# Kernel optimization log

Hardware: AMD Instinct MI355X
Metric: run time of the kernel (lower is better)

## Reference

```python
import jax, jax.numpy as jnp
import numpy as np


def setup_inputs() -> dict:
    key = jax.random.key(0)
    ks = jax.random.split(key, 5)
    B, C, H, W = 4, 256, 64, 64
    Cq = C // 8
    x = jax.random.normal(ks[0], (B, C, H, W), dtype=jnp.float32)
    Wq = jax.random.normal(ks[1], (Cq, C), dtype=jnp.float32) * (1.0 / np.sqrt(C))
    Wk = jax.random.normal(ks[2], (Cq, C), dtype=jnp.float32) * (1.0 / np.sqrt(C))
    Wv = jax.random.normal(ks[3], (C, C), dtype=jnp.float32) * (1.0 / np.sqrt(C))
    bq = jnp.zeros((Cq,), dtype=jnp.float32)
    bk = jnp.zeros((Cq,), dtype=jnp.float32)
    bv = jnp.zeros((C,), dtype=jnp.float32)
    gamma = jnp.ones((1,), dtype=jnp.float32)
    return {"x": x, "Wq": Wq, "bq": bq, "Wk": Wk, "bk": bk, "Wv": Wv, "bv": bv, "gamma": gamma}


def reference(x, Wq, bq, Wk, bk, Wv, bv, gamma):
    B, C, H, W = x.shape
    N = H * W
    xf = x.reshape(B, C, N)                      # (B, C, N)
    # 1x1 convs == per-pixel linear projections over channels
    q = jnp.einsum('dc,bcn->bdn', Wq, xf) + bq[None, :, None]   # (B, C/8, N)
    k = jnp.einsum('dc,bcn->bdn', Wk, xf) + bk[None, :, None]   # (B, C/8, N)
    v = jnp.einsum('dc,bcn->bdn', Wv, xf) + bv[None, :, None]   # (B, C,   N)
    # attention: note original has NO 1/sqrt(d) scaling
    scores = jnp.einsum('bdn,bdm->bnm', q, k)     # (B, N, N)
    attn = jax.nn.softmax(scores, axis=-1)
    out = jnp.einsum('bnm,bdm->bnd', attn, v)     # (B, N, C)
    out = out.transpose(0, 2, 1).reshape(B, C, H, W)
    return gamma * out + x
```

## Files before the change

kernel.cpp:

```cpp
#include <hip/hip_runtime.h>

#define BATCH 4
#define CH    256
#define DQ    32
#define NPIX  4096
#define LOG2E 1.4426950408889634f

typedef unsigned short u16;
typedef unsigned int   u32;
typedef __attribute__((ext_vector_type(8))) short short8;
typedef __attribute__((ext_vector_type(16))) float f32x16;

#if defined(__has_builtin)
#if __has_builtin(__builtin_amdgcn_exp2f)
#define EXP2F(x) __builtin_amdgcn_exp2f(x)
#else
#define EXP2F(x) __expf((x) * 0.6931471805599453f)
#endif
#else
#define EXP2F(x) __expf((x) * 0.6931471805599453f)
#endif

__device__ __forceinline__ float b2f(u32 u) {
  union { u32 i; float f; } v; v.i = (u & 0xffffu) << 16; return v.f;
}
__device__ __forceinline__ u16 f2b(float f) {
  union { float f; u32 i; } v; v.f = f;
  u32 x = v.i; x += 0x7fffu + ((x >> 16) & 1u);
  return (u16)(x >> 16);
}
__device__ __forceinline__ u32 pack_hi16(float lo, float hi) {
  union { float f; u32 i; } a, b; a.f = lo; b.f = hi;
  return __builtin_amdgcn_perm(b.i, a.i, 0x07060302u);
}

__global__ __launch_bounds__(256) void wconv(
    const float* __restrict__ Wq, const float* __restrict__ Wk,
    const float* __restrict__ Wv, u16* __restrict__ wsz, u16* __restrict__ wsz_lo)
{
  const int blk = blockIdx.x;
  const int jt = blk >> 4, kk = blk & 15;
  #pragma unroll
  for (int rep = 0; rep < 2; ++rep) {
    const int idx = rep * 256 + threadIdx.x;
    const int j = idx >> 4, el = idx & 15, e = kk * 16 + el;
    const float* Wsrc = (jt == 0) ? Wq : (jt == 1) ? Wk : Wv;
    const int row = (jt <= 1) ? j : (jt - 2) * 32 + j;
    float v = Wsrc[(size_t)row * CH + e];
    if (jt == 0) v *= LOG2E;
    const u16 hi = f2b(v);
    const int o = (((jt * 16 + kk) * 2 + (el >> 3)) * 32 + j) * 8 + (el & 7);
    wsz[o] = hi;
    if (jt < 2) wsz_lo[o] = f2b(v - b2f(hi));
  }
}

__global__ __launch_bounds__(64, 4) void proj(
    const float* __restrict__ x,
    const u16* __restrict__ wsz, const u16* __restrict__ wsz_lo,
    const float* __restrict__ bq, const float* __restrict__ bk, const float* __restrict__ bv,
    u16* __restrict__ q_t, u16* __restrict__ k_t, u16* __restrict__ v_swz)
{
  const int nt = blockIdx.x, jt = blockIdx.y, b = blockIdx.z;
  const int lane = threadIdx.x & 63, hl = lane >> 5, l31 = lane & 31;
  const int n = nt * 32 + l31;

  const float* xb = x + (size_t)b * CH * NPIX + n;

  if (jt <= 1) {
    f32x16 a0, a1, a2;
    #pragma unroll
    for (int r = 0; r < 16; ++r) { a0[r] = 0.f; a1[r] = 0.f; a2[r] = 0.f; }
    for (int kk = 0; kk < 16; ++kk) {
      const int wo = ((jt * 16 + kk) * 2 + hl) * 256 + l31 * 8;
      const short8 Ah = *(const short8*)&wsz[wo];
      const short8 Al = *(const short8*)&wsz_lo[wo];
      float xv[8];
      #pragma unroll
      for (int j = 0; j < 8; ++j)
        xv[j] = xb[(size_t)(kk * 16 + hl * 8 + j) * NPIX];
      union { u32 u[4]; short8 s; } Bh, Bl;
      #pragma unroll
      for (int j2 = 0; j2 < 4; ++j2) {
        const u16 h0 = f2b(xv[2 * j2]),     h1 = f2b(xv[2 * j2 + 1]);
        const u16 l0 = f2b(xv[2 * j2] - b2f(h0));
        const u16 l1 = f2b(xv[2 * j2 + 1] - b2f(h1));
        Bh.u[j2] = (u32)h0 | ((u32)h1 << 16);
        Bl.u[j2] = (u32)l0 | ((u32)l1 << 16);
      }
      a0 = __builtin_amdgcn_mfma_f32_32x32x16_bf16(Ah, Bh.s, a0, 0, 0, 0);
      a1 = __builtin_amdgcn_mfma_f32_32x32x16_bf16(Ah, Bl.s, a1, 0, 0, 0);
      a2 = __builtin_amdgcn_mfma_f32_32x32x16_bf16(Al, Bh.s, a2, 0, 0, 0);
    }
    u16* dst = (jt == 0) ? q_t : k_t;
    const float* bias = (jt == 0) ? bq : bk;
    const float bscale = (jt == 0) ? LOG2E : 1.0f;
    #pragma unroll
    for (int r = 0; r < 16; ++r) {
      const int d = (r & 3) + 8 * (r >> 2) + 4 * hl;
      dst[((size_t)b * NPIX + n) * DQ + d] =
        f2b((a0[r] + a1[r]) + (a2[r] + bias[d] * bscale));
    }
  } else {
    f32x16 a0, a1;
    #pragma unroll
    for (int r = 0; r < 16; ++r) { a0[r] = 0.f; a1[r] = 0.f; }
    for (int kk = 0; kk < 16; kk += 2) {
      #pragma unroll
      for (int par = 0; par < 2; ++par) {
        const int k2 = kk + par;
        const short8 Ah = *(const short8*)&wsz[((jt * 16 + k2) * 2 + hl) * 256 + l31 * 8];
        float xv[8];
        #pragma unroll
        for (int j = 0; j < 8; ++j)
          xv[j] = xb[(size_t)(k2 * 16 + hl * 8 + j) * NPIX];
        union { u32 u[4]; short8 s; } Bh;
        #pragma unroll
        for (int j2 = 0; j2 < 4; ++j2)
          Bh.u[j2] = (u32)f2b(xv[2 * j2]) | ((u32)f2b(xv[2 * j2 + 1]) << 16);
        if (par == 0) a0 = __builtin_amdgcn_mfma_f32_32x32x16_bf16(Ah, Bh.s, a0, 0, 0, 0);
        else          a1 = __builtin_amdgcn_mfma_f32_32x32x16_bf16(Ah, Bh.s, a1, 0, 0, 0);
      }
    }
    const int ctv = jt - 2;
    const int kc = (l31 >> 4) & 1, h3 = (l31 >> 3) & 1, j8 = l31 & 7;
    u16* dst = v_swz + (((((size_t)b * 128 + nt) * 8 + ctv) * 2 + kc) * 2 + h3) * 256 + j8;
    #pragma unroll
    for (int r = 0; r < 16; ++r) {
      const int c5 = (r & 3) + 8 * (r >> 2) + 4 * hl;
      dst[c5 * 8] = f2b(a0[r] + a1[r] + bv[ctv * 32 + c5]);
    }
  }
}

__global__ __launch_bounds__(512, 1) void attn(
    const u16* __restrict__ q_t, const u16* __restrict__ k_t,
    const u16* __restrict__ v_swz, const float* __restrict__ x,
    const float* __restrict__ gamma, float* __restrict__ out)
{
  const int b = blockIdx.y, t = threadIdx.x;
  const int w = t >> 6, lane = t & 63, hl = lane >> 5, l31 = lane & 31;
  const int mq = w >> 1, ch = w & 1;
  const int n0 = blockIdx.x * 64;

  __shared__ float cbuf[16384];
  __shared__ float lbuf[8][2][64];

  short8 qf[2][2];
  #pragma unroll
  for (int nt = 0; nt < 2; ++nt)
    #pragma unroll
    for (int kd = 0; kd < 2; ++kd)
      qf[nt][kd] = *(const short8*)(q_t + ((size_t)b * NPIX + n0 + nt * 32 + l31) * DQ + kd * 16 + hl * 8);

  f32x16 acc[8];
  #pragma unroll
  for (int a = 0; a < 8; ++a)
    #pragma unroll
    for (int r = 0; r < 16; ++r) acc[a][r] = 0.f;
  float lrun[2] = {0.f, 0.f};

  const u16* kb = k_t + (size_t)b * NPIX * DQ;
  const u16* vb = v_swz + (size_t)b * 128 * 8192;

  for (int cc = 0; cc < 32; ++cc) {
    const int mc = mq * 32 + cc;

    const u16* kp = kb + (size_t)(mc * 32 + l31) * DQ + hl * 8;
    const short8 kf0 = *(const short8*)(kp);
    const short8 kf1 = *(const short8*)(kp + 16);

    short8 av[4][2];
    const u16* vp = vb + (size_t)mc * 8192 + (size_t)hl * 256 + l31 * 8;
    #pragma unroll
    for (int ct = 0; ct < 4; ++ct)
      #pragma unroll
      for (int kc = 0; kc < 2; ++kc)
        av[ct][kc] = *(const short8*)(vp + (((ch * 4 + ct) * 2 + kc) * 2) * 256);

    union { uint4 u; short8 s; } bu[2][2];
    #pragma unroll
    for (int nt = 0; nt < 2; ++nt) {
      f32x16 st;
      #pragma unroll
      for (int r = 0; r < 16; ++r) st[r] = 0.f;
      st = __builtin_amdgcn_mfma_f32_32x32x16_bf16(kf0, qf[nt][0], st, 0, 0, 0);
      st = __builtin_amdgcn_mfma_f32_32x32x16_bf16(kf1, qf[nt][1], st, 0, 0, 0);
      u32 pk[4][2];
      #pragma unroll
      for (int g = 0; g < 4; ++g) {
        const float e0 = EXP2F(st[4 * g + 0]);
        const float e1 = EXP2F(st[4 * g + 1]);
        const float e2 = EXP2F(st[4 * g + 2]);
        const float e3 = EXP2F(st[4 * g + 3]);
        lrun[nt] += (e0 + e1) + (e2 + e3);
        pk[g][0] = pack_hi16(e0, e1);
        pk[g][1] = pack_hi16(e2, e3);
      }
      #pragma unroll
      for (int kc = 0; kc < 2; ++kc) {
        const u32 s0 = hl ? pk[2 * kc][0] : pk[2 * kc + 1][0];
        const u32 s1 = hl ? pk[2 * kc][1] : pk[2 * kc + 1][1];
        const u32 r0 = (u32)__shfl_xor((int)s0, 32);
        const u32 r1 = (u32)__shfl_xor((int)s1, 32);
        bu[nt][kc].u.x = hl ? r0 : pk[2 * kc][0];
        bu[nt][kc].u.y = hl ? r1 : pk[2 * kc][1];
        bu[nt][kc].u.z = hl ? pk[2 * kc + 1][0] : r0;
        bu[nt][kc].u.w = hl ? pk[2 * kc + 1][1] : r1;
      }
    }

    #pragma unroll
    for (int kc = 0; kc < 2; ++kc)
      #pragma unroll
      for (int ct = 0; ct < 4; ++ct)
        #pragma unroll
        for (int nt = 0; nt < 2; ++nt)
          acc[nt * 4 + ct] =
            __builtin_amdgcn_mfma_f32_32x32x16_bf16(av[ct][kc], bu[nt][kc].s, acc[nt * 4 + ct], 0, 0, 0);
  }

  lbuf[w][0][lane] = lrun[0];
  lbuf[w][1][lane] = lrun[1];

  #pragma unroll
  for (int nt = 0; nt < 2; ++nt) {
    if (mq == 1 || mq == 3) {
      const int slot = (ch * 2 + (mq >> 1)) * 4096;
      #pragma unroll
      for (int ct = 0; ct < 4; ++ct)
        #pragma unroll
        for (int r = 0; r < 16; ++r)
          cbuf[slot + (ct * 16 + r) * 64 + lane] = acc[nt * 4 + ct][r];
    }
    __syncthreads();
    if (mq == 0 || mq == 2) {
      const int slot = (ch * 2 + (mq >> 1)) * 4096;
      #pragma unroll
      for (int ct = 0; ct < 4; ++ct)
        #pragma unroll
        for (int r = 0; r < 16; ++r)
          acc[nt * 4 + ct][r] += cbuf[slot + (ct * 16 + r) * 64 + lane];
    }
    __syncthreads();
    if (mq == 2) {
      const int slot = ch * 2 * 4096;
      #pragma unroll
      for (int ct = 0; ct < 4; ++ct)
        #pragma unroll
        for (int r = 0; r < 16; ++r)
          cbuf[slot + (ct * 16 + r) * 64 + lane] = acc[nt * 4 + ct][r];
    }
    __syncthreads();
    if (mq == 0) {
      const int slot = ch * 2 * 4096;
      #pragma unroll
      for (int ct = 0; ct < 4; ++ct)
        #pragma unroll
        for (int r = 0; r < 16; ++r)
          acc[nt * 4 + ct][r] += cbuf[slot + (ct * 16 + r) * 64 + lane];
    }
    __syncthreads();
  }

  if (mq == 0) {
    const float g = gamma[0];
    #pragma unroll
    for (int nt = 0; nt < 2; ++nt) {
      float l = 0.f;
      #pragma unroll
      for (int ww = 0; ww < 8; ++ww) l += lbuf[ww][nt][lane];
      l += __shfl_xor(l, 32);
      const float linv = 2.0f / l;
      #pragma unroll
      for (int ct = 0; ct < 4; ++ct)
        #pragma unroll
        for (int r = 0; r < 16; ++r) {
          const int c = (ch * 4 + ct) * 32 + (r & 3) + 8 * (r >> 2) + 4 * hl;
          const size_t idx = ((size_t)b * CH + c) * NPIX + n0 + nt * 32 + l31;
          out[idx] = g * acc[nt * 4 + ct][r] * linv + x[idx];
        }
    }
  }
}

extern "C" void kernel_launch(void* const* d_in, const int* in_sizes, int n_in,
                              void* d_out, int out_size, void* d_ws, size_t ws_size,
                              hipStream_t stream) {
  const float* x  = (const float*)d_in[0];
  const float* Wq = (const float*)d_in[1];
  const float* bq = (const float*)d_in[2];
  const float* Wk = (const float*)d_in[3];
  const float* bk = (const float*)d_in[4];
  const float* Wv = (const float*)d_in[5];
  const float* bv = (const float*)d_in[6];
  const float* gm = (const float*)d_in[7];
  float* out = (float*)d_out;

  const size_t qk_e = (size_t)BATCH * NPIX * DQ;
  const size_t v_e  = (size_t)BATCH * NPIX * CH;
  const size_t w_e  = 10 * 16 * 2 * 32 * 8;
  const size_t wl_e = 2 * 16 * 2 * 32 * 8;
  const size_t need = (2 * qk_e + v_e + w_e + wl_e) * sizeof(u16);
  if (ws_size < need) return;

  u16* q_t    = (u16*)d_ws;
  u16* k_t    = q_t + qk_e;
  u16* v_swz  = k_t + qk_e;
  u16* wsz    = v_swz + v_e;
  u16* wsz_lo = wsz + w_e;

  wconv<<<dim3(160), 256, 0, stream>>>(Wq, Wk, Wv, wsz, wsz_lo);
  proj <<<dim3(NPIX / 32, 10, BATCH), 64, 0, stream>>>(x, wsz, wsz_lo, bq, bk, bv, q_t, k_t, v_swz);
  attn <<<dim3(NPIX / 64, BATCH), 512, 0, stream>>>(q_t, k_t, v_swz, x, gm, out);
}
```

Measured before the change: 184.8 us.

## Stage x tile in LDS once per block in projection; split V loads in attention

The projection kernel now launches one 256-thread block per pixel tile and batch instead of ten 64-thread blocks. It loads the x tile once with float4 reads, converts it to bf16 hi/lo in shared memory, and all four waves reuse it for the Q, K and V outputs. This removes the tenfold redundant strided global reads of x and repeated bf16 conversion, at the cost of LDS use and fewer, heavier blocks. In the attention kernel the V fragment loads are split into two halves interleaved with the MFMAs, lowering register pressure.

```diff
diff --git a/kernel.cpp b/kernel.cpp
--- a/kernel.cpp
+++ b/kernel.cpp
@@ -55,42 +55,52 @@
   }
 }
 
-__global__ __launch_bounds__(64, 4) void proj(
+__global__ __launch_bounds__(256) void proj(
     const float* __restrict__ x,
     const u16* __restrict__ wsz, const u16* __restrict__ wsz_lo,
     const float* __restrict__ bq, const float* __restrict__ bk, const float* __restrict__ bv,
     u16* __restrict__ q_t, u16* __restrict__ k_t, u16* __restrict__ v_swz)
 {
-  const int nt = blockIdx.x, jt = blockIdx.y, b = blockIdx.z;
-  const int lane = threadIdx.x & 63, hl = lane >> 5, l31 = lane & 31;
-  const int n = nt * 32 + l31;
-
-  const float* xb = x + (size_t)b * CH * NPIX + n;
-
-  if (jt <= 1) {
+  const int nt = blockIdx.x, b = blockIdx.y;
+  const int n0 = nt * 32;
+  const int t = threadIdx.x;
+  const int w = t >> 6, hl = (t >> 5) & 1, l31 = t & 31;
+
+  __shared__ __align__(16) u16 xh[32 * 264];
+  __shared__ __align__(16) u16 xl[32 * 264];
+
+  #pragma unroll
+  for (int p = 0; p < 8; ++p) {
+    const int e = p * 32 + (t >> 3), n4 = (t & 7) * 4;
+    const float4 v4 = *(const float4*)&x[((size_t)b * CH + e) * NPIX + n0 + n4];
+    const float vv[4] = {v4.x, v4.y, v4.z, v4.w};
+    #pragma unroll
+    for (int jj = 0; jj < 4; ++jj) {
+      const u16 hi = f2b(vv[jj]);
+      xh[(n4 + jj) * 264 + e] = hi;
+      xl[(n4 + jj) * 264 + e] = f2b(vv[jj] - b2f(hi));
+    }
+  }
+  __syncthreads();
+
+  const int n = n0 + l31;
+
+  if (w <= 1) {
+    const int jt = w;
     f32x16 a0, a1, a2;
     #pragma unroll
     for (int r = 0; r < 16; ++r) { a0[r] = 0.f; a1[r] = 0.f; a2[r] = 0.f; }
+    #pragma unroll
     for (int kk = 0; kk < 16; ++kk) {
       const int wo = ((jt * 16 + kk) * 2 + hl) * 256 + l31 * 8;
       const short8 Ah = *(const short8*)&wsz[wo];
       const short8 Al = *(const short8*)&wsz_lo[wo];
-      float xv[8];
-      #pragma unroll
-      for (int j = 0; j < 8; ++j)
-        xv[j] = xb[(size_t)(kk * 16 + hl * 8 + j) * NPIX];
-      union { u32 u[4]; short8 s; } Bh, Bl;
-      #pragma unroll
-      for (int j2 = 0; j2 < 4; ++j2) {
-        const u16 h0 = f2b(xv[2 * j2]),     h1 = f2b(xv[2 * j2 + 1]);
-        const u16 l0 = f2b(xv[2 * j2] - b2f(h0));
-        const u16 l1 = f2b(xv[2 * j2 + 1] - b2f(h1));
-        Bh.u[j2] = (u32)h0 | ((u32)h1 << 16);
-        Bl.u[j2] = (u32)l0 | ((u32)l1 << 16);
-      }
-      a0 = __builtin_amdgcn_mfma_f32_32x32x16_bf16(Ah, Bh.s, a0, 0, 0, 0);
-      a1 = __builtin_amdgcn_mfma_f32_32x32x16_bf16(Ah, Bl.s, a1, 0, 0, 0);
-      a2 = __builtin_amdgcn_mfma_f32_32x32x16_bf16(Al, Bh.s, a2, 0, 0, 0);
+      const int xo = l31 * 264 + kk * 16 + hl * 8;
+      const short8 Bh = *(const short8*)&xh[xo];
+      const short8 Bl = *(const short8*)&xl[xo];
+      a0 = __builtin_amdgcn_mfma_f32_32x32x16_bf16(Ah, Bh, a0, 0, 0, 0);
+      a1 = __builtin_amdgcn_mfma_f32_32x32x16_bf16(Ah, Bl, a1, 0, 0, 0);
+      a2 = __builtin_amdgcn_mfma_f32_32x32x16_bf16(Al, Bh, a2, 0, 0, 0);
     }
     u16* dst = (jt == 0) ? q_t : k_t;
     const float* bias = (jt == 0) ? bq : bk;
@@ -102,33 +112,29 @@
         f2b((a0[r] + a1[r]) + (a2[r] + bias[d] * bscale));
     }
   } else {
-    f32x16 a0, a1;
-    #pragma unroll
-    for (int r = 0; r < 16; ++r) { a0[r] = 0.f; a1[r] = 0.f; }
-    for (int kk = 0; kk < 16; kk += 2) {
-      #pragma unroll
-      for (int par = 0; par < 2; ++par) {
-        const int k2 = kk + par;
-        const short8 Ah = *(const short8*)&wsz[((jt * 16 + k2) * 2 + hl) * 256 + l31 * 8];
-        float xv[8];
-        #pragma unroll
-        for (int j = 0; j < 8; ++j)
-          xv[j] = xb[(size_t)(k2 * 16 + hl * 8 + j) * NPIX];
-        union { u32 u[4]; short8 s; } Bh;
-        #pragma unroll
-        for (int j2 = 0; j2 < 4; ++j2)
-          Bh.u[j2] = (u32)f2b(xv[2 * j2]) | ((u32)f2b(xv[2 * j2 + 1]) << 16);
-        if (par == 0) a0 = __builtin_amdgcn_mfma_f32_32x32x16_bf16(Ah, Bh.s, a0, 0, 0, 0);
-        else          a1 = __builtin_amdgcn_mfma_f32_32x32x16_bf16(Ah, Bh.s, a1, 0, 0, 0);
+    #pragma unroll
+    for (int ci = 0; ci < 4; ++ci) {
+      const int ctv = (w - 2) * 4 + ci;
+      const int jt = 2 + ctv;
+      f32x16 a0, a1;
+      #pragma unroll
+      for (int r = 0; r < 16; ++r) { a0[r] = 0.f; a1[r] = 0.f; }
+      #pragma unroll
+      for (int kk = 0; kk < 16; kk += 2) {
+        const short8 Ah0 = *(const short8*)&wsz[((jt * 16 + kk) * 2 + hl) * 256 + l31 * 8];
+        const short8 Bh0 = *(const short8*)&xh[l31 * 264 + kk * 16 + hl * 8];
+        const short8 Ah1 = *(const short8*)&wsz[((jt * 16 + kk + 1) * 2 + hl) * 256 + l31 * 8];
+        const short8 Bh1 = *(const short8*)&xh[l31 * 264 + (kk + 1) * 16 + hl * 8];
+        a0 = __builtin_amdgcn_mfma_f32_32x32x16_bf16(Ah0, Bh0, a0, 0, 0, 0);
+        a1 = __builtin_amdgcn_mfma_f32_32x32x16_bf16(Ah1, Bh1, a1, 0, 0, 0);
       }
-    }
-    const int ctv = jt - 2;
-    const int kc = (l31 >> 4) & 1, h3 = (l31 >> 3) & 1, j8 = l31 & 7;
-    u16* dst = v_swz + (((((size_t)b * 128 + nt) * 8 + ctv) * 2 + kc) * 2 + h3) * 256 + j8;
-    #pragma unroll
-    for (int r = 0; r < 16; ++r) {
-      const int c5 = (r & 3) + 8 * (r >> 2) + 4 * hl;
-      dst[c5 * 8] = f2b(a0[r] + a1[r] + bv[ctv * 32 + c5]);
+      const int kc = (l31 >> 4) & 1, h3 = (l31 >> 3) & 1, j8 = l31 & 7;
+      u16* dst = v_swz + (((((size_t)b * 128 + nt) * 8 + ctv) * 2 + kc) * 2 + h3) * 256 + j8;
+      #pragma unroll
+      for (int r = 0; r < 16; ++r) {
+        const int c5 = (r & 3) + 8 * (r >> 2) + 4 * hl;
+        dst[c5 * 8] = f2b(a0[r] + a1[r] + bv[ctv * 32 + c5]);
+      }
     }
   }
 }
@@ -170,13 +176,11 @@
     const short8 kf0 = *(const short8*)(kp);
     const short8 kf1 = *(const short8*)(kp + 16);
 
-    short8 av[4][2];
     const u16* vp = vb + (size_t)mc * 8192 + (size_t)hl * 256 + l31 * 8;
+    short8 av[4];
     #pragma unroll
     for (int ct = 0; ct < 4; ++ct)
-      #pragma unroll
-      for (int kc = 0; kc < 2; ++kc)
-        av[ct][kc] = *(const short8*)(vp + (((ch * 4 + ct) * 2 + kc) * 2) * 256);
+      av[ct] = *(const short8*)(vp + (((ch * 4 + ct) * 2 + 0) * 2) * 256);
 
     union { uint4 u; short8 s; } bu[2][2];
     #pragma unroll
@@ -211,13 +215,21 @@
     }
 
     #pragma unroll
-    for (int kc = 0; kc < 2; ++kc)
-      #pragma unroll
-      for (int ct = 0; ct < 4; ++ct)
-        #pragma unroll
-        for (int nt = 0; nt < 2; ++nt)
-          acc[nt * 4 + ct] =
-            __builtin_amdgcn_mfma_f32_32x32x16_bf16(av[ct][kc], bu[nt][kc].s, acc[nt * 4 + ct], 0, 0, 0);
+    for (int ct = 0; ct < 4; ++ct)
+      #pragma unroll
+      for (int nt = 0; nt < 2; ++nt)
+        acc[nt * 4 + ct] =
+          __builtin_amdgcn_mfma_f32_32x32x16_bf16(av[ct], bu[nt][0].s, acc[nt * 4 + ct], 0, 0, 0);
+
+    #pragma unroll
+    for (int ct = 0; ct < 4; ++ct)
+      av[ct] = *(const short8*)(vp + (((ch * 4 + ct) * 2 + 1) * 2) * 256);
+    #pragma unroll
+    for (int ct = 0; ct < 4; ++ct)
+      #pragma unroll
+      for (int nt = 0; nt < 2; ++nt)
+        acc[nt * 4 + ct] =
+          __builtin_amdgcn_mfma_f32_32x32x16_bf16(av[ct], bu[nt][1].s, acc[nt * 4 + ct], 0, 0, 0);
   }
 
   lbuf[w][0][lane] = lrun[0];
@@ -311,6 +323,6 @@
   u16* wsz_lo = wsz + w_e;
 
   wconv<<<dim3(160), 256, 0, stream>>>(Wq, Wk, Wv, wsz, wsz_lo);
-  proj <<<dim3(NPIX / 32, 10, BATCH), 64, 0, stream>>>(x, wsz, wsz_lo, bq, bk, bv, q_t, k_t, v_swz);
+  proj <<<dim3(NPIX / 32, BATCH), 256, 0, stream>>>(x, wsz, wsz_lo, bq, bk, bv, q_t, k_t, v_swz);
   attn <<<dim3(NPIX / 64, BATCH), 512, 0, stream>>>(q_t, k_t, v_swz, x, gm, out);
 }
```

Result: slower. 188.6 us (+2.0%).
